# Optimization experiments

Hardware: AMD Instinct MI355X
Metric: run time of the kernel (lower is better)

The kernel has to match this reference:

```python
import jax, jax.numpy as jnp
import numpy as np

B, T, C = 4, 2048, 1024
H, D, CS = 16, 64, 16   # heads, head dim, titans chunk size
EPS = 1e-5


def setup_inputs():
    key = jax.random.key(0)
    ks = jax.random.split(key, 4)
    s = 0.02
    return {
        "x": jax.random.normal(ks[0], (B, T, C), jnp.float32),
        "W_attn": jax.random.normal(ks[1], (C, 3 * C), jnp.float32) * s,
        "b_attn": jnp.zeros((3 * C,), jnp.float32),
        "W_param": jax.random.normal(ks[2], (C, 3 * H), jnp.float32) * s,
        "b_param": jnp.zeros((3 * H,), jnp.float32),
        "W_proj": jax.random.normal(ks[3], (C, C), jnp.float32) * s,
        "b_proj": jnp.zeros((C,), jnp.float32),
        "w": jnp.ones((H, D), jnp.float32),
        "b": jnp.zeros((H, D), jnp.float32),
    }


def _ln(x, w, b):
    # per-head layernorm over last dim
    mu = x.mean(-1, keepdims=True)
    xc = x - mu
    rstd = jax.lax.rsqrt((xc * xc).mean(-1, keepdims=True) + EPS)
    return xc * rstd * w + b


def _ln_bwd(x, w, dy):
    # gradient of layernorm(x; w, b) w.r.t. x, given upstream dy
    mu = x.mean(-1, keepdims=True)
    xc = x - mu
    rstd = jax.lax.rsqrt((xc * xc).mean(-1, keepdims=True) + EPS)
    xhat = xc * rstd
    wdy = dy * w
    c1 = (xhat * wdy).mean(-1, keepdims=True)
    c2 = wdy.mean(-1, keepdims=True)
    return (wdy - xhat * c1 - c2) * rstd


def _chunk_titans_linear(q, k, v, w, b, theta, alpha, eta):
    # q,k,v: [B,H,T,D]; theta/alpha/eta: [B,H,T,1]; w,b: [H,D]
    NT = T // CS
    wr = w.reshape(1, H, 1, D)
    br = b.reshape(1, H, 1, D)

    def to_chunks(t):
        return t.reshape(B, H, NT, CS, t.shape[-1]).transpose(2, 0, 1, 3, 4)

    qc, kc, vc = to_chunks(q), to_chunks(k), to_chunks(v)
    tc, ac, ec = to_chunks(theta), to_chunks(alpha), to_chunks(eta)

    def chunk_step(carry, inp):
        S, m = carry  # memory state / momentum: [B,H,D,D]
        q_i, k_i, v_i, th_i, al_i, et_i = inp
        # gradients of ||LN(k S) - v||^2 w.r.t. S, taken at the chunk-start state
        kh = jnp.einsum('bhcd,bhde->bhce', k_i, S)
        d_recon = 2.0 * (_ln(kh, wr, br) - v_i)
        dkh = _ln_bwd(kh, wr, d_recon)
        grads = jnp.einsum('bhci,bhcj->bhcij', k_i, dkh)  # [B,H,CS,D,D]

        def tok_step(c2, t_inp):
            S_t, m_t = c2
            g, th, al, et = t_inp
            th = th[..., None]; al = al[..., None]; et = et[..., None]
            m_t = et * m_t - th * g          # momentum
            S_t = (1.0 - al) * S_t + m_t     # weight-decayed state update
            return (S_t, m_t), S_t

        (S, m), S_seq = jax.lax.scan(
            tok_step, (S, m),
            (grads.transpose(2, 0, 1, 3, 4),
             th_i.transpose(2, 0, 1, 3),
             al_i.transpose(2, 0, 1, 3),
             et_i.transpose(2, 0, 1, 3)))
        # read memory with the freshly updated per-token state
        o_i = jnp.einsum('bhcd,cbhde->bhce', q_i, S_seq)
        return (S, m), o_i

    S0 = jnp.zeros((B, H, D, D), q.dtype)
    m0 = jnp.zeros((B, H, D, D), q.dtype)
    _, o_chunks = jax.lax.scan(chunk_step, (S0, m0), (qc, kc, vc, tc, ac, ec))
    o = o_chunks.transpose(1, 2, 0, 3, 4).reshape(B, H, T, D)
    return _ln(o, wr, br)  # normalized memory readout


def reference(x, W_attn, b_attn, W_param, b_param, W_proj, b_proj, w, b):
    qkv = x @ W_attn + b_attn
    q, k, v = jnp.split(qkv, 3, axis=-1)

    def heads(t):
        return t.reshape(B, T, H, D).transpose(0, 2, 1, 3)

    q, k, v = heads(q), heads(k), heads(v)
    q = q / jnp.maximum(jnp.linalg.norm(q, axis=-1, keepdims=True), 1e-12)
    k = k / jnp.maximum(jnp.linalg.norm(k, axis=-1, keepdims=True), 1e-12)
    p = jax.nn.sigmoid((x @ W_param + b_param).reshape(B, T, H, 3).transpose(0, 2, 1, 3))
    theta, alpha, eta = p[..., 0:1], p[..., 1:2], p[..., 2:3]
    o = _chunk_titans_linear(q, k, v, w, b, theta, alpha, eta)
    o = o.transpose(0, 2, 1, 3).reshape(B, T, C)
    return o @ W_proj + b_proj
```

## Files before the change

kernel.cpp:

```cpp
#include <hip/hip_runtime.h>
#include <cstddef>
#include <cstdint>
#include <math.h>

#define BB   4
#define TT   2048
#define CCH  1024
#define HH   16
#define DD   64
#define CSZ  16
#define NTC  128
#define EPSF 1e-5f
#define WVS  8

typedef __attribute__((ext_vector_type(8))) short bf16x8;
typedef __attribute__((ext_vector_type(4))) float f32x4;
typedef __attribute__((ext_vector_type(2))) float f32x2;

__device__ __forceinline__ void bar_lds() {
  asm volatile("s_waitcnt lgkmcnt(0)" ::: "memory");
  __builtin_amdgcn_s_barrier();
}

__device__ __forceinline__ uint32_t pack_split(float f) {
  uint32_t b = __float_as_uint(f);
  uint32_t uh = (b + 0x7fffu + ((b >> 16) & 1u)) >> 16;
  float fh = __uint_as_float(uh << 16);
  float r = f - fh;
  return uh | (__float_as_uint(r) & 0xffff0000u);
}
__device__ __forceinline__ float unpack_f(uint32_t u) {
  return __uint_as_float(u << 16) + __uint_as_float(u & 0xffff0000u);
}

__device__ __forceinline__ float wave_sum(float x) {
  float v = x;
  v += __int_as_float(__builtin_amdgcn_update_dpp(0, __float_as_int(v), 0x111, 0xf, 0xf, true));
  v += __int_as_float(__builtin_amdgcn_update_dpp(0, __float_as_int(v), 0x112, 0xf, 0xf, true));
  v += __int_as_float(__builtin_amdgcn_update_dpp(0, __float_as_int(v), 0x114, 0xf, 0xf, true));
  v += __int_as_float(__builtin_amdgcn_update_dpp(0, __float_as_int(v), 0x118, 0xf, 0xf, true));
  v += __int_as_float(__builtin_amdgcn_update_dpp(0, __float_as_int(v), 0x142, 0xa, 0xf, true));
  v += __int_as_float(__builtin_amdgcn_update_dpp(0, __float_as_int(v), 0x143, 0xc, 0xf, true));
  return __int_as_float(__builtin_amdgcn_readlane(__float_as_int(v), 63));
}

__device__ __forceinline__ float sigmoidf_(float x) {
  return 1.f / (1.f + expf(-x));
}

__global__ __launch_bounds__(256) void split_transpose(
    const float* __restrict__ W, uint32_t* __restrict__ Wt, int K, int N) {
  __shared__ float t[32][33];
  const int n0 = blockIdx.x * 32, k0 = blockIdx.y * 32;
  const int tx = threadIdx.x & 31, ty = threadIdx.x >> 5;
#pragma unroll
  for (int i = 0; i < 4; i++)
    t[ty + i * 8][tx] = W[(size_t)(k0 + ty + i * 8) * N + n0 + tx];
  __syncthreads();
#pragma unroll
  for (int i = 0; i < 4; i++)
    Wt[(size_t)(n0 + ty + i * 8) * K + k0 + tx] = pack_split(t[tx][ty + i * 8]);
}

template<bool A_PACKED, bool C_PACKED>
__global__ __launch_bounds__(256) void gemm_split(
    const void* __restrict__ Av, int lda,
    const uint32_t* __restrict__ Bt,
    const float* __restrict__ bias,
    void* __restrict__ Cv, int M, int N, int K) {
  __shared__ unsigned short Ahi[128][40];
  __shared__ unsigned short Alo[128][40];
  __shared__ unsigned short Bhi[128][40];
  __shared__ unsigned short Blo[128][40];

  const int tid = threadIdx.x;
  const int row0 = blockIdx.y * 128;
  const int col0 = blockIdx.x * 128;
  const int wv = tid >> 6;
  const int l  = tid & 63;
  const int wr = wv >> 1, wc = wv & 1;
  const int lrow = l & 15;
  const int kgrp = (l >> 4) * 8;

  const int sr = tid >> 1;
  const int sk = (tid & 1) * 16;

  f32x4 acc[4][4];
#pragma unroll
  for (int i = 0; i < 4; i++)
#pragma unroll
    for (int j = 0; j < 4; j++) acc[i][j] = (f32x4){0.f, 0.f, 0.f, 0.f};

  uint4 pa[4];
  float4 pf[4];
  uint4 pb[4];

  auto load_tile = [&](int k0) {
    if (A_PACKED) {
      const uint32_t* Ap = (const uint32_t*)Av + (size_t)(row0 + sr) * lda + k0 + sk;
#pragma unroll
      for (int i = 0; i < 4; i++) pa[i] = *(const uint4*)(Ap + i * 4);
    } else {
      const float* Ap = (const float*)Av + (size_t)(row0 + sr) * lda + k0 + sk;
#pragma unroll
      for (int i = 0; i < 4; i++) pf[i] = *(const float4*)(Ap + i * 4);
    }
    const uint32_t* Bp = Bt + (size_t)(col0 + sr) * K + k0 + sk;
#pragma unroll
    for (int i = 0; i < 4; i++) pb[i] = *(const uint4*)(Bp + i * 4);
  };

  auto commit_tile = [&]() {
    uint32_t hp[8], lp[8];
    if (A_PACKED) {
      uint32_t u[16];
#pragma unroll
      for (int i = 0; i < 4; i++) *(uint4*)&u[i * 4] = pa[i];
#pragma unroll
      for (int j = 0; j < 8; j++) {
        hp[j] = (u[2 * j] & 0xffffu) | (u[2 * j + 1] << 16);
        lp[j] = (u[2 * j] >> 16) | (u[2 * j + 1] & 0xffff0000u);
      }
    } else {
      float f[16];
#pragma unroll
      for (int i = 0; i < 4; i++) *(float4*)&f[i * 4] = pf[i];
      uint32_t uh[16], ulr[16];
#pragma unroll
      for (int j = 0; j < 16; j++) {
        uint32_t b = __float_as_uint(f[j]);
        uint32_t h = (b + 0x7fffu + ((b >> 16) & 1u)) >> 16;
        uh[j] = h;
        ulr[j] = __float_as_uint(f[j] - __uint_as_float(h << 16));
      }
#pragma unroll
      for (int j = 0; j < 8; j++) {
        hp[j] = uh[2 * j] | (uh[2 * j + 1] << 16);
        lp[j] = (ulr[2 * j] >> 16) | (ulr[2 * j + 1] & 0xffff0000u);
      }
    }
    *(uint4*)&Ahi[sr][sk]     = *(uint4*)&hp[0];
    *(uint4*)&Ahi[sr][sk + 8] = *(uint4*)&hp[4];
    *(uint4*)&Alo[sr][sk]     = *(uint4*)&lp[0];
    *(uint4*)&Alo[sr][sk + 8] = *(uint4*)&lp[4];
    {
      uint32_t u[16], bh[8], bl[8];
#pragma unroll
      for (int i = 0; i < 4; i++) *(uint4*)&u[i * 4] = pb[i];
#pragma unroll
      for (int j = 0; j < 8; j++) {
        bh[j] = (u[2 * j] & 0xffffu) | (u[2 * j + 1] << 16);
        bl[j] = (u[2 * j] >> 16) | (u[2 * j + 1] & 0xffff0000u);
      }
      *(uint4*)&Bhi[sr][sk]     = *(uint4*)&bh[0];
      *(uint4*)&Bhi[sr][sk + 8] = *(uint4*)&bh[4];
      *(uint4*)&Blo[sr][sk]     = *(uint4*)&bl[0];
      *(uint4*)&Blo[sr][sk + 8] = *(uint4*)&bl[4];
    }
  };

  load_tile(0);
  for (int k0 = 0; k0 < K; k0 += 32) {
    commit_tile();
    bar_lds();
    if (k0 + 32 < K) load_tile(k0 + 32);

    bf16x8 bh[4], bl[4];
#pragma unroll
    for (int j = 0; j < 4; j++) {
      bh[j] = *(const bf16x8*)&Bhi[wc * 64 + j * 16 + lrow][kgrp];
      bl[j] = *(const bf16x8*)&Blo[wc * 64 + j * 16 + lrow][kgrp];
    }
#pragma unroll
    for (int i = 0; i < 4; i++) {
      bf16x8 ah = *(const bf16x8*)&Ahi[wr * 64 + i * 16 + lrow][kgrp];
      bf16x8 al = *(const bf16x8*)&Alo[wr * 64 + i * 16 + lrow][kgrp];
#pragma unroll
      for (int j = 0; j < 4; j++) {
        acc[i][j] = __builtin_amdgcn_mfma_f32_16x16x32_bf16(ah, bh[j], acc[i][j], 0, 0, 0);
        acc[i][j] = __builtin_amdgcn_mfma_f32_16x16x32_bf16(ah, bl[j], acc[i][j], 0, 0, 0);
        acc[i][j] = __builtin_amdgcn_mfma_f32_16x16x32_bf16(al, bh[j], acc[i][j], 0, 0, 0);
      }
    }
    bar_lds();
  }

  const int crow4 = (l >> 4) * 4;
#pragma unroll
  for (int i = 0; i < 4; i++) {
#pragma unroll
    for (int j = 0; j < 4; j++) {
      const int col = col0 + wc * 64 + j * 16 + lrow;
      const float bv = bias[col];
      const int rowb = row0 + wr * 64 + i * 16 + crow4;
#pragma unroll
      for (int r = 0; r < 4; r++) {
        float v = acc[i][j][r] + bv;
        size_t off = (size_t)(rowb + r) * N + col;
        if (C_PACKED) ((uint32_t*)Cv)[off] = pack_split(v);
        else          ((float*)Cv)[off] = v;
      }
    }
  }
}

__global__ __launch_bounds__(256) void gemm_f32(
    const float* __restrict__ A, int lda,
    const float* __restrict__ W,
    const float* __restrict__ bias,
    float* __restrict__ C, int M, int N, int K) {
  __shared__ float As[16][132];
  __shared__ float Bs[16][128];
  const int tid  = threadIdx.x;
  const int row0 = blockIdx.y * 128;
  const int col0 = blockIdx.x * 128;
  const int ty = tid >> 4;
  const int tx = tid & 15;
  const int a_r = tid >> 2;
  const int a_k = (tid & 3) << 2;
  const int b_r = tid >> 5;
  const int b_c = (tid & 31) << 2;

  float acc[8][8];
#pragma unroll
  for (int i = 0; i < 8; i++)
#pragma unroll
    for (int j = 0; j < 8; j++) acc[i][j] = 0.f;

  float4 areg[2], breg[2];
  const int gc = col0 + b_c;
#pragma unroll
  for (int i = 0; i < 2; i++)
    areg[i] = *(const float4*)(A + (size_t)(row0 + a_r + i * 64) * lda + a_k);
#pragma unroll
  for (int i = 0; i < 2; i++) {
    breg[i] = make_float4(0.f, 0.f, 0.f, 0.f);
    if (gc < N) breg[i] = *(const float4*)(W + (size_t)(b_r + i * 8) * N + gc);
  }

  for (int k0 = 0; k0 < K; k0 += 16) {
#pragma unroll
    for (int i = 0; i < 2; i++) {
      int r = a_r + i * 64;
      As[a_k + 0][r] = areg[i].x;
      As[a_k + 1][r] = areg[i].y;
      As[a_k + 2][r] = areg[i].z;
      As[a_k + 3][r] = areg[i].w;
    }
#pragma unroll
    for (int i = 0; i < 2; i++) *(float4*)(&Bs[b_r + i * 8][b_c]) = breg[i];
    bar_lds();

    if (k0 + 16 < K) {
#pragma unroll
      for (int i = 0; i < 2; i++)
        areg[i] = *(const float4*)(A + (size_t)(row0 + a_r + i * 64) * lda + (k0 + 16 + a_k));
#pragma unroll
      for (int i = 0; i < 2; i++) {
        breg[i] = make_float4(0.f, 0.f, 0.f, 0.f);
        if (gc < N) breg[i] = *(const float4*)(W + (size_t)(k0 + 16 + b_r + i * 8) * N + gc);
      }
    }

#pragma unroll
    for (int kk = 0; kk < 16; kk++) {
      float af[8], bf[8];
      *(float4*)&af[0] = *(const float4*)&As[kk][ty * 8];
      *(float4*)&af[4] = *(const float4*)&As[kk][ty * 8 + 4];
      *(float4*)&bf[0] = *(const float4*)&Bs[kk][tx * 8];
      *(float4*)&bf[4] = *(const float4*)&Bs[kk][tx * 8 + 4];
#pragma unroll
      for (int i = 0; i < 8; i++)
#pragma unroll
        for (int j = 0; j < 8; j++) acc[i][j] += af[i] * bf[j];
    }
    bar_lds();
  }
#pragma unroll
  for (int i = 0; i < 8; i++) {
    int r = row0 + ty * 8 + i;
#pragma unroll
    for (int j0 = 0; j0 < 8; j0 += 4) {
      int cc = col0 + tx * 8 + j0;
      if (cc < N) {
        float4 ov;
        ov.x = acc[i][j0 + 0] + bias[cc + 0];
        ov.y = acc[i][j0 + 1] + bias[cc + 1];
        ov.z = acc[i][j0 + 2] + bias[cc + 2];
        ov.w = acc[i][j0 + 3] + bias[cc + 3];
        *(float4*)(C + (size_t)r * N + cc) = ov;
      }
    }
  }
}

__global__ __launch_bounds__(256) void normalize_qk(uint32_t* __restrict__ qkv) {
  const int idx = blockIdx.x * 4 + (threadIdx.x >> 6);
  const int l = threadIdx.x & 63;
  const int rowBT = idx >> 5;
  const int rem = idx & 31;
  const int which = rem >> 4;
  const int h = rem & 15;
  const size_t addr = (size_t)rowBT * 3072 + (size_t)which * 1024 + h * 64 + l;
  float v = unpack_f(qkv[addr]);
  float ss = wave_sum(v * v);
  float sc = 1.f / fmaxf(sqrtf(ss), 1e-12f);
  qkv[addr] = pack_split(v * sc);
}

__global__ __launch_bounds__(512) void titans_rec(
    uint32_t* __restrict__ qkv, const float* __restrict__ p,
    const float* __restrict__ w, const float* __restrict__ bparm) {
  const int bh = blockIdx.x;
  const int b = bh >> 4;
  const int h = bh & 15;
  const int tid = threadIdx.x;
  const int wv = tid >> 6;
  const int l = tid & 63;

  __shared__ float k_s[2][CSZ][DD];
  __shared__ float q_s[2][CSZ][DD];
  __shared__ float v_s[CSZ][DD];
  __shared__ float dkh_s[CSZ][DD];
  __shared__ float part[2][WVS][CSZ][DD];
  __shared__ float4 prm_s[2][CSZ];

  f32x2 S2[4], M2[4];
#pragma unroll
  for (int r = 0; r < 4; r++) { S2[r] = (f32x2){0.f, 0.f}; M2[r] = (f32x2){0.f, 0.f}; }

  const float w_l = w[h * DD + l];
  const float b_l = bparm[h * DD + l];

  uint32_t* qbase = qkv + (size_t)(b * TT) * 3072 + h * DD;
  const float* pbase = p + (size_t)(b * TT) * 48 + h * 3;

  uint32_t rq[2], rk[2], rv[2];
  float rp0 = 0.f, rp1 = 0.f, rp2 = 0.f;
  {
#pragma unroll
    for (int i = 0; i < 2; i++) {
      const int row = wv + i * 8;
      size_t roff = (size_t)row * 3072 + l;
      q_s[0][row][l] = unpack_f(qbase[roff]);
      k_s[0][row][l] = unpack_f(qbase[roff + 1024]);
      v_s[row][l]    = unpack_f(qbase[roff + 2048]);
    }
    if (tid < CSZ) {
      const float* pp = pbase + (size_t)tid * 48;
      prm_s[0][tid] = make_float4(sigmoidf_(pp[0]), sigmoidf_(pp[1]), sigmoidf_(pp[2]), 0.f);
    }
#pragma unroll
    for (int i = 0; i < 2; i++) {
      size_t roff = (size_t)(CSZ + wv + i * 8) * 3072 + l;
      rq[i] = qbase[roff];
      rk[i] = qbase[roff + 1024];
      rv[i] = qbase[roff + 2048];
    }
    if (tid < CSZ) {
      const float* pp = pbase + (size_t)(CSZ + tid) * 48;
      rp0 = pp[0]; rp1 = pp[1]; rp2 = pp[2];
    }
  }
  bar_lds();

  for (int nt = 0; nt < NTC; nt++) {
    const int buf = nt & 1;
    float (*partw)[CSZ][DD] = part[buf];
    float (*partr)[CSZ][DD] = part[buf ^ 1];

    if (nt > 0) {
#pragma unroll
      for (int i = 0; i < 2; i++) {
        const int t = wv + i * 8;
        float o = 0.f;
#pragma unroll
        for (int ww = 0; ww < WVS; ww++) o += partr[ww][t][l];
        float mu = wave_sum(o) * (1.f / 64.f);
        float xc = o - mu;
        float var = wave_sum(xc * xc) * (1.f / 64.f);
        float rstd = rsqrtf(var + EPSF);
        float y = xc * rstd * w_l + b_l;
        qbase[(size_t)((nt - 1) * CSZ + t) * 3072 + 2048 + l] = pack_split(y);
      }
    }
#pragma unroll
    for (int c = 0; c < CSZ; c++) {
      const f32x2* kp2 = (const f32x2*)&k_s[buf][c][wv * 8];
      f32x2 a2;
      a2 = kp2[0] * S2[0];
      a2 = kp2[1] * S2[1] + a2;
      a2 = kp2[2] * S2[2] + a2;
      a2 = kp2[3] * S2[3] + a2;
      partw[wv][c][l] = a2.x + a2.y;
    }
    bar_lds();

#pragma unroll
    for (int i = 0; i < 2; i++) {
      const int c = wv + i * 8;
      float kh = 0.f;
#pragma unroll
      for (int ww = 0; ww < WVS; ww++) kh += partw[ww][c][l];
      float mu = wave_sum(kh) * (1.f / 64.f);
      float xc = kh - mu;
      float var = wave_sum(xc * xc) * (1.f / 64.f);
      float rstd = rsqrtf(var + EPSF);
      float xhat = xc * rstd;
      float y = xhat * w_l + b_l;
      float dy = 2.f * (y - v_s[c][l]);
      float wdy = dy * w_l;
      float c1 = wave_sum(xhat * wdy) * (1.f / 64.f);
      float c2 = wave_sum(wdy) * (1.f / 64.f);
      dkh_s[c][l] = (wdy - xhat * c1 - c2) * rstd;
    }
    bar_lds();

    if (nt + 1 < NTC) {
#pragma unroll
      for (int i = 0; i < 2; i++) {
        const int row = wv + i * 8;
        k_s[buf ^ 1][row][l] = unpack_f(rk[i]);
        q_s[buf ^ 1][row][l] = unpack_f(rq[i]);
        v_s[row][l] = unpack_f(rv[i]);
      }
      if (tid < CSZ)
        prm_s[buf ^ 1][tid] = make_float4(sigmoidf_(rp0), sigmoidf_(rp1), sigmoidf_(rp2), 0.f);
    }
    if (nt + 2 < NTC) {
#pragma unroll
      for (int i = 0; i < 2; i++) {
        size_t roff = (size_t)((nt + 2) * CSZ + wv + i * 8) * 3072 + l;
        rq[i] = qbase[roff];
        rk[i] = qbase[roff + 1024];
        rv[i] = qbase[roff + 2048];
      }
      if (tid < CSZ) {
        const float* pp = pbase + (size_t)((nt + 2) * CSZ + tid) * 48;
        rp0 = pp[0]; rp1 = pp[1]; rp2 = pp[2];
      }
    }
#pragma unroll
    for (int t = 0; t < CSZ; t++) {
      float4 prm = prm_s[buf][t];
      float a = prm.x * dkh_s[t][l];
      const f32x2 na2 = (f32x2){-a, -a};
      const f32x2 et2 = (f32x2){prm.z, prm.z};
      const f32x2 be2 = (f32x2){1.f - prm.y, 1.f - prm.y};
      const f32x2* kp2 = (const f32x2*)&k_s[buf][t][wv * 8];
      const f32x2* qp2 = (const f32x2*)&q_s[buf][t][wv * 8];
      f32x2 po2 = (f32x2){0.f, 0.f};
#pragma unroll
      for (int pq = 0; pq < 4; pq++) {
        M2[pq] = et2 * M2[pq] + na2 * kp2[pq];
        S2[pq] = be2 * S2[pq] + M2[pq];
        po2    = qp2[pq] * S2[pq] + po2;
      }
      partw[wv][t][l] = po2.x + po2.y;
    }
    bar_lds();
  }

  {
    float (*partr)[CSZ][DD] = part[(NTC - 1) & 1];
#pragma unroll
    for (int i = 0; i < 2; i++) {
      const int t = wv + i * 8;
      float o = 0.f;
#pragma unroll
      for (int ww = 0; ww < WVS; ww++) o += partr[ww][t][l];
      float mu = wave_sum(o) * (1.f / 64.f);
      float xc = o - mu;
      float var = wave_sum(xc * xc) * (1.f / 64.f);
      float rstd = rsqrtf(var + EPSF);
      float y = xc * rstd * w_l + b_l;
      qbase[(size_t)((NTC - 1) * CSZ + t) * 3072 + 2048 + l] = pack_split(y);
    }
  }
}

extern "C" void kernel_launch(void* const* d_in, const int* in_sizes, int n_in,
                              void* d_out, int out_size, void* d_ws, size_t ws_size,
                              hipStream_t stream) {
  const float* x      = (const float*)d_in[0];
  const float* W_attn = (const float*)d_in[1];
  const float* b_attn = (const float*)d_in[2];
  const float* W_parm = (const float*)d_in[3];
  const float* b_parm = (const float*)d_in[4];
  const float* W_proj = (const float*)d_in[5];
  const float* b_proj = (const float*)d_in[6];
  const float* w      = (const float*)d_in[7];
  const float* bb     = (const float*)d_in[8];
  float* out = (float*)d_out;

  const int M = BB * TT;
  float* qkv = (float*)d_ws;
  float* pbf = qkv + (size_t)M * 3072;
  uint32_t* wattn_t = (uint32_t*)(pbf + (size_t)M * 48);
  uint32_t* wproj_t = wattn_t + (size_t)3072 * 1024;

  split_transpose<<<dim3(3072 / 32, 1024 / 32), 256, 0, stream>>>(W_attn, wattn_t, 1024, 3072);
  split_transpose<<<dim3(1024 / 32, 1024 / 32), 256, 0, stream>>>(W_proj, wproj_t, 1024, 1024);

  gemm_split<false, true><<<dim3(3072 / 128, M / 128), 256, 0, stream>>>(
      x, CCH, wattn_t, b_attn, qkv, M, 3072, CCH);
  gemm_f32<<<dim3(1, M / 128), 256, 0, stream>>>(x, CCH, W_parm, b_parm, pbf, M, 48, CCH);
  normalize_qk<<<(M * 2 * HH) / 4, 256, 0, stream>>>((uint32_t*)qkv);
  titans_rec<<<BB * HH, 512, 0, stream>>>((uint32_t*)qkv, pbf, w, bb);
  gemm_split<true, false><<<dim3(CCH / 128, M / 128), 256, 0, stream>>>(
      (uint32_t*)qkv + 2048, 3072, wproj_t, b_proj, out, M, CCH, CCH);
}
```

Before: 977.4 us.

## Fuse param projection and q/k normalization into the QKV split GEMM

Appends the 48 gate-parameter columns to the transposed QKV weight so a single split-bf16 GEMM produces q, k, v and raw gate logits into one strided buffer. The separate fp32 param GEMM goes away, and so does the separate q/k L2-normalization pass, which now runs in the GEMM epilogue through a 16-lane DPP reduction. The recurrence kernel reads the gate values from the new wider row stride. In exchange the fused GEMM launches an extra mostly-empty column tile, the gate logits come out of the bf16-split MMA path rather than plain fp32, and two device memcpys are added to concatenate the biases.

```diff
diff --git a/kernel.cpp b/kernel.cpp
--- a/kernel.cpp
+++ b/kernel.cpp
@@ -12,6 +12,7 @@
 #define NTC  128
 #define EPSF 1e-5f
 #define WVS  8
+#define STR  3120
 
 typedef __attribute__((ext_vector_type(8))) short bf16x8;
 typedef __attribute__((ext_vector_type(4))) float f32x4;
@@ -44,30 +45,44 @@
   return __int_as_float(__builtin_amdgcn_readlane(__float_as_int(v), 63));
 }
 
+__device__ __forceinline__ float red16(float x) {
+  float v = x;
+  v += __int_as_float(__builtin_amdgcn_update_dpp(0, __float_as_int(v), 0x0B1, 0xf, 0xf, true));
+  v += __int_as_float(__builtin_amdgcn_update_dpp(0, __float_as_int(v), 0x04E, 0xf, 0xf, true));
+  v += __int_as_float(__builtin_amdgcn_update_dpp(0, __float_as_int(v), 0x124, 0xf, 0xf, true));
+  v += __int_as_float(__builtin_amdgcn_update_dpp(0, __float_as_int(v), 0x128, 0xf, 0xf, true));
+  return v;
+}
+
 __device__ __forceinline__ float sigmoidf_(float x) {
   return 1.f / (1.f + expf(-x));
 }
 
 __global__ __launch_bounds__(256) void split_transpose(
-    const float* __restrict__ W, uint32_t* __restrict__ Wt, int K, int N) {
+    const float* __restrict__ W, uint32_t* __restrict__ Wt, int K, int N, int rowOff) {
   __shared__ float t[32][33];
   const int n0 = blockIdx.x * 32, k0 = blockIdx.y * 32;
   const int tx = threadIdx.x & 31, ty = threadIdx.x >> 5;
 #pragma unroll
-  for (int i = 0; i < 4; i++)
-    t[ty + i * 8][tx] = W[(size_t)(k0 + ty + i * 8) * N + n0 + tx];
+  for (int i = 0; i < 4; i++) {
+    int n = n0 + tx;
+    t[ty + i * 8][tx] = (n < N) ? W[(size_t)(k0 + ty + i * 8) * N + n] : 0.f;
+  }
   __syncthreads();
 #pragma unroll
-  for (int i = 0; i < 4; i++)
-    Wt[(size_t)(n0 + ty + i * 8) * K + k0 + tx] = pack_split(t[tx][ty + i * 8]);
-}
-
-template<bool A_PACKED, bool C_PACKED>
+  for (int i = 0; i < 4; i++) {
+    int n = n0 + ty + i * 8;
+    if (n < N)
+      Wt[(size_t)(rowOff + n) * K + k0 + tx] = pack_split(t[tx][ty + i * 8]);
+  }
+}
+
+template<bool A_PACKED, bool C_PACKED, bool NORM>
 __global__ __launch_bounds__(256) void gemm_split(
     const void* __restrict__ Av, int lda,
     const uint32_t* __restrict__ Bt,
     const float* __restrict__ bias,
-    void* __restrict__ Cv, int M, int N, int K) {
+    void* __restrict__ Cv, int M, int ldc, int K, int Nb, int Ns, int pklim) {
   __shared__ unsigned short Ahi[128][40];
   __shared__ unsigned short Alo[128][40];
   __shared__ unsigned short Bhi[128][40];
@@ -105,9 +120,14 @@
 #pragma unroll
       for (int i = 0; i < 4; i++) pf[i] = *(const float4*)(Ap + i * 4);
     }
-    const uint32_t* Bp = Bt + (size_t)(col0 + sr) * K + k0 + sk;
-#pragma unroll
-    for (int i = 0; i < 4; i++) pb[i] = *(const uint4*)(Bp + i * 4);
+    if (col0 + sr < Nb) {
+      const uint32_t* Bp = Bt + (size_t)(col0 + sr) * K + k0 + sk;
+#pragma unroll
+      for (int i = 0; i < 4; i++) pb[i] = *(const uint4*)(Bp + i * 4);
+    } else {
+#pragma unroll
+      for (int i = 0; i < 4; i++) pb[i] = make_uint4(0u, 0u, 0u, 0u);
+    }
   };
 
   auto commit_tile = [&]() {
@@ -186,130 +206,59 @@
   }
 
   const int crow4 = (l >> 4) * 4;
-#pragma unroll
-  for (int i = 0; i < 4; i++) {
-#pragma unroll
-    for (int j = 0; j < 4; j++) {
-      const int col = col0 + wc * 64 + j * 16 + lrow;
-      const float bv = bias[col];
-      const int rowb = row0 + wr * 64 + i * 16 + crow4;
+  if (NORM && col0 < 2048) {
+    float bj[4];
+#pragma unroll
+    for (int j = 0; j < 4; j++) bj[j] = bias[col0 + wc * 64 + j * 16 + lrow];
+#pragma unroll
+    for (int i = 0; i < 4; i++) {
 #pragma unroll
       for (int r = 0; r < 4; r++) {
-        float v = acc[i][j][r] + bv;
-        size_t off = (size_t)(rowb + r) * N + col;
-        if (C_PACKED) ((uint32_t*)Cv)[off] = pack_split(v);
-        else          ((float*)Cv)[off] = v;
-      }
-    }
-  }
-}
-
-__global__ __launch_bounds__(256) void gemm_f32(
-    const float* __restrict__ A, int lda,
-    const float* __restrict__ W,
-    const float* __restrict__ bias,
-    float* __restrict__ C, int M, int N, int K) {
-  __shared__ float As[16][132];
-  __shared__ float Bs[16][128];
-  const int tid  = threadIdx.x;
-  const int row0 = blockIdx.y * 128;
-  const int col0 = blockIdx.x * 128;
-  const int ty = tid >> 4;
-  const int tx = tid & 15;
-  const int a_r = tid >> 2;
-  const int a_k = (tid & 3) << 2;
-  const int b_r = tid >> 5;
-  const int b_c = (tid & 31) << 2;
-
-  float acc[8][8];
-#pragma unroll
-  for (int i = 0; i < 8; i++)
-#pragma unroll
-    for (int j = 0; j < 8; j++) acc[i][j] = 0.f;
-
-  float4 areg[2], breg[2];
-  const int gc = col0 + b_c;
-#pragma unroll
-  for (int i = 0; i < 2; i++)
-    areg[i] = *(const float4*)(A + (size_t)(row0 + a_r + i * 64) * lda + a_k);
-#pragma unroll
-  for (int i = 0; i < 2; i++) {
-    breg[i] = make_float4(0.f, 0.f, 0.f, 0.f);
-    if (gc < N) breg[i] = *(const float4*)(W + (size_t)(b_r + i * 8) * N + gc);
-  }
-
-  for (int k0 = 0; k0 < K; k0 += 16) {
-#pragma unroll
-    for (int i = 0; i < 2; i++) {
-      int r = a_r + i * 64;
-      As[a_k + 0][r] = areg[i].x;
-      As[a_k + 1][r] = areg[i].y;
-      As[a_k + 2][r] = areg[i].z;
-      As[a_k + 3][r] = areg[i].w;
-    }
-#pragma unroll
-    for (int i = 0; i < 2; i++) *(float4*)(&Bs[b_r + i * 8][b_c]) = breg[i];
-    bar_lds();
-
-    if (k0 + 16 < K) {
-#pragma unroll
-      for (int i = 0; i < 2; i++)
-        areg[i] = *(const float4*)(A + (size_t)(row0 + a_r + i * 64) * lda + (k0 + 16 + a_k));
-#pragma unroll
-      for (int i = 0; i < 2; i++) {
-        breg[i] = make_float4(0.f, 0.f, 0.f, 0.f);
-        if (gc < N) breg[i] = *(const float4*)(W + (size_t)(k0 + 16 + b_r + i * 8) * N + gc);
-      }
-    }
-
-#pragma unroll
-    for (int kk = 0; kk < 16; kk++) {
-      float af[8], bf[8];
-      *(float4*)&af[0] = *(const float4*)&As[kk][ty * 8];
-      *(float4*)&af[4] = *(const float4*)&As[kk][ty * 8 + 4];
-      *(float4*)&bf[0] = *(const float4*)&Bs[kk][tx * 8];
-      *(float4*)&bf[4] = *(const float4*)&Bs[kk][tx * 8 + 4];
-#pragma unroll
-      for (int i = 0; i < 8; i++)
-#pragma unroll
-        for (int j = 0; j < 8; j++) acc[i][j] += af[i] * bf[j];
-    }
-    bar_lds();
-  }
-#pragma unroll
-  for (int i = 0; i < 8; i++) {
-    int r = row0 + ty * 8 + i;
-#pragma unroll
-    for (int j0 = 0; j0 < 8; j0 += 4) {
-      int cc = col0 + tx * 8 + j0;
-      if (cc < N) {
-        float4 ov;
-        ov.x = acc[i][j0 + 0] + bias[cc + 0];
-        ov.y = acc[i][j0 + 1] + bias[cc + 1];
-        ov.z = acc[i][j0 + 2] + bias[cc + 2];
-        ov.w = acc[i][j0 + 3] + bias[cc + 3];
-        *(float4*)(C + (size_t)r * N + cc) = ov;
-      }
-    }
-  }
-}
-
-__global__ __launch_bounds__(256) void normalize_qk(uint32_t* __restrict__ qkv) {
-  const int idx = blockIdx.x * 4 + (threadIdx.x >> 6);
-  const int l = threadIdx.x & 63;
-  const int rowBT = idx >> 5;
-  const int rem = idx & 31;
-  const int which = rem >> 4;
-  const int h = rem & 15;
-  const size_t addr = (size_t)rowBT * 3072 + (size_t)which * 1024 + h * 64 + l;
-  float v = unpack_f(qkv[addr]);
-  float ss = wave_sum(v * v);
-  float sc = 1.f / fmaxf(sqrtf(ss), 1e-12f);
-  qkv[addr] = pack_split(v * sc);
+        float vals[4];
+        float ss = 0.f;
+#pragma unroll
+        for (int j = 0; j < 4; j++) {
+          vals[j] = acc[i][j][r] + bj[j];
+          ss += vals[j] * vals[j];
+        }
+        ss = red16(ss);
+        float sc = 1.f / fmaxf(sqrtf(ss), 1e-12f);
+        const int rowb = row0 + wr * 64 + i * 16 + crow4 + r;
+#pragma unroll
+        for (int j = 0; j < 4; j++) {
+          const int col = col0 + wc * 64 + j * 16 + lrow;
+          ((uint32_t*)Cv)[(size_t)rowb * ldc + col] = pack_split(vals[j] * sc);
+        }
+      }
+    }
+  } else {
+#pragma unroll
+    for (int i = 0; i < 4; i++) {
+#pragma unroll
+      for (int j = 0; j < 4; j++) {
+        const int col = col0 + wc * 64 + j * 16 + lrow;
+        const float bv = (col < Ns) ? bias[col] : 0.f;
+        const int rowb = row0 + wr * 64 + i * 16 + crow4;
+#pragma unroll
+        for (int r = 0; r < 4; r++) {
+          float v = acc[i][j][r] + bv;
+          size_t off = (size_t)(rowb + r) * ldc + col;
+          if (col < Ns) {
+            if (C_PACKED) {
+              uint32_t word = (col < pklim) ? pack_split(v) : __float_as_uint(v);
+              ((uint32_t*)Cv)[off] = word;
+            } else {
+              ((float*)Cv)[off] = v;
+            }
+          }
+        }
+      }
+    }
+  }
 }
 
 __global__ __launch_bounds__(512) void titans_rec(
-    uint32_t* __restrict__ qkv, const float* __restrict__ p,
+    uint32_t* __restrict__ qkv,
     const float* __restrict__ w, const float* __restrict__ bparm) {
   const int bh = blockIdx.x;
   const int b = bh >> 4;
@@ -332,8 +281,8 @@
   const float w_l = w[h * DD + l];
   const float b_l = bparm[h * DD + l];
 
-  uint32_t* qbase = qkv + (size_t)(b * TT) * 3072 + h * DD;
-  const float* pbase = p + (size_t)(b * TT) * 48 + h * 3;
+  uint32_t* qbase = qkv + (size_t)(b * TT) * STR + h * DD;
+  const float* pbase = (const float*)qkv + (size_t)(b * TT) * STR + 3072 + h * 3;
 
   uint32_t rq[2], rk[2], rv[2];
   float rp0 = 0.f, rp1 = 0.f, rp2 = 0.f;
@@ -341,24 +290,24 @@
 #pragma unroll
     for (int i = 0; i < 2; i++) {
       const int row = wv + i * 8;
-      size_t roff = (size_t)row * 3072 + l;
+      size_t roff = (size_t)row * STR + l;
       q_s[0][row][l] = unpack_f(qbase[roff]);
       k_s[0][row][l] = unpack_f(qbase[roff + 1024]);
       v_s[row][l]    = unpack_f(qbase[roff + 2048]);
     }
     if (tid < CSZ) {
-      const float* pp = pbase + (size_t)tid * 48;
+      const float* pp = pbase + (size_t)tid * STR;
       prm_s[0][tid] = make_float4(sigmoidf_(pp[0]), sigmoidf_(pp[1]), sigmoidf_(pp[2]), 0.f);
     }
 #pragma unroll
     for (int i = 0; i < 2; i++) {
-      size_t roff = (size_t)(CSZ + wv + i * 8) * 3072 + l;
+      size_t roff = (size_t)(CSZ + wv + i * 8) * STR + l;
       rq[i] = qbase[roff];
       rk[i] = qbase[roff + 1024];
       rv[i] = qbase[roff + 2048];
     }
     if (tid < CSZ) {
-      const float* pp = pbase + (size_t)(CSZ + tid) * 48;
+      const float* pp = pbase + (size_t)(CSZ + tid) * STR;
       rp0 = pp[0]; rp1 = pp[1]; rp2 = pp[2];
     }
   }
@@ -381,7 +330,7 @@
         float var = wave_sum(xc * xc) * (1.f / 64.f);
         float rstd = rsqrtf(var + EPSF);
         float y = xc * rstd * w_l + b_l;
-        qbase[(size_t)((nt - 1) * CSZ + t) * 3072 + 2048 + l] = pack_split(y);
+        qbase[(size_t)((nt - 1) * CSZ + t) * STR + 2048 + l] = pack_split(y);
       }
     }
 #pragma unroll
@@ -430,13 +379,13 @@
     if (nt + 2 < NTC) {
 #pragma unroll
       for (int i = 0; i < 2; i++) {
-        size_t roff = (size_t)((nt + 2) * CSZ + wv + i * 8) * 3072 + l;
+        size_t roff = (size_t)((nt + 2) * CSZ + wv + i * 8) * STR + l;
         rq[i] = qbase[roff];
         rk[i] = qbase[roff + 1024];
         rv[i] = qbase[roff + 2048];
       }
       if (tid < CSZ) {
-        const float* pp = pbase + (size_t)((nt + 2) * CSZ + tid) * 48;
+        const float* pp = pbase + (size_t)((nt + 2) * CSZ + tid) * STR;
         rp0 = pp[0]; rp1 = pp[1]; rp2 = pp[2];
       }
     }
@@ -474,7 +423,7 @@
       float var = wave_sum(xc * xc) * (1.f / 64.f);
       float rstd = rsqrtf(var + EPSF);
       float y = xc * rstd * w_l + b_l;
-      qbase[(size_t)((NTC - 1) * CSZ + t) * 3072 + 2048 + l] = pack_split(y);
+      qbase[(size_t)((NTC - 1) * CSZ + t) * STR + 2048 + l] = pack_split(y);
     }
   }
 }
@@ -494,19 +443,21 @@
   float* out = (float*)d_out;
 
   const int M = BB * TT;
-  float* qkv = (float*)d_ws;
-  float* pbf = qkv + (size_t)M * 3072;
-  uint32_t* wattn_t = (uint32_t*)(pbf + (size_t)M * 48);
-  uint32_t* wproj_t = wattn_t + (size_t)3072 * 1024;
-
-  split_transpose<<<dim3(3072 / 32, 1024 / 32), 256, 0, stream>>>(W_attn, wattn_t, 1024, 3072);
-  split_transpose<<<dim3(1024 / 32, 1024 / 32), 256, 0, stream>>>(W_proj, wproj_t, 1024, 1024);
-
-  gemm_split<false, true><<<dim3(3072 / 128, M / 128), 256, 0, stream>>>(
-      x, CCH, wattn_t, b_attn, qkv, M, 3072, CCH);
-  gemm_f32<<<dim3(1, M / 128), 256, 0, stream>>>(x, CCH, W_parm, b_parm, pbf, M, 48, CCH);
-  normalize_qk<<<(M * 2 * HH) / 4, 256, 0, stream>>>((uint32_t*)qkv);
-  titans_rec<<<BB * HH, 512, 0, stream>>>((uint32_t*)qkv, pbf, w, bb);
-  gemm_split<true, false><<<dim3(CCH / 128, M / 128), 256, 0, stream>>>(
-      (uint32_t*)qkv + 2048, 3072, wproj_t, b_proj, out, M, CCH, CCH);
-}
+  uint32_t* qkv     = (uint32_t*)d_ws;
+  uint32_t* wattn_t = qkv + (size_t)M * STR;
+  uint32_t* wproj_t = wattn_t + (size_t)3120 * 1024;
+  float*    bcat    = (float*)(wproj_t + (size_t)1024 * 1024);
+
+  hipMemcpyAsync(bcat, b_attn, 3072 * sizeof(float), hipMemcpyDeviceToDevice, stream);
+  hipMemcpyAsync(bcat + 3072, b_parm, 48 * sizeof(float), hipMemcpyDeviceToDevice, stream);
+
+  split_transpose<<<dim3(3072 / 32, 1024 / 32), 256, 0, stream>>>(W_attn, wattn_t, 1024, 3072, 0);
+  split_transpose<<<dim3(2, 1024 / 32), 256, 0, stream>>>(W_parm, wattn_t, 1024, 48, 3072);
+  split_transpose<<<dim3(1024 / 32, 1024 / 32), 256, 0, stream>>>(W_proj, wproj_t, 1024, 1024, 0);
+
+  gemm_split<false, true, true><<<dim3(25, M / 128), 256, 0, stream>>>(
+      x, CCH, wattn_t, bcat, qkv, M, STR, CCH, 3120, 3120, 3072);
+  titans_rec<<<BB * HH, 512, 0, stream>>>(qkv, w, bb);
+  gemm_split<true, false, false><<<dim3(CCH / 128, M / 128), 256, 0, stream>>>(
+      qkv + 2048, STR, wproj_t, b_proj, out, M, CCH, CCH, 1024, 1024, 0);
+}
```

New measurement: 954.6 us. 1.02x faster.
